# Performance work log

Measured on AMD Instinct MI355X. Metric: run time of the kernel, lower is better.

Reference implementation:

```python
import jax, jax.numpy as jnp
import numpy as np
import math

L, B, E, H = 1024, 4, 1024, 16
HD = E // H

def setup_inputs() -> dict:
    key = jax.random.key(0)
    ks = jax.random.split(key, 8)
    bound_in = math.sqrt(6.0 / (3 * E + E))  # xavier_uniform for [3E, E]
    bound_out = math.sqrt(1.0 / E)           # default Linear init
    return {
        "query": jax.random.normal(ks[0], (L, B, E), jnp.float32),
        "key": jax.random.normal(ks[1], (L, B, E), jnp.float32),
        "value": jax.random.normal(ks[2], (L, B, E), jnp.float32),
        "attn_mask": jnp.zeros((B, L, L), jnp.float32),
        "in_proj_weight": jax.random.uniform(ks[3], (3 * E, E), jnp.float32, -bound_in, bound_in),
        "in_proj_bias": jnp.zeros((3 * E,), jnp.float32),
        "out_proj_weight": jax.random.uniform(ks[4], (E, E), jnp.float32, -bound_out, bound_out),
        "out_proj_bias": jnp.zeros((E,), jnp.float32),
    }

def reference(query, key, value, attn_mask, in_proj_weight, in_proj_bias,
              out_proj_weight, out_proj_bias):
    # packed in-projection: q/k/v [L, B, E]
    q = query @ in_proj_weight[:E].T + in_proj_bias[:E]
    k = key @ in_proj_weight[E:2 * E].T + in_proj_bias[E:2 * E]
    v = value @ in_proj_weight[2 * E:].T + in_proj_bias[2 * E:]
    # [L, B, E] -> [B*H, L, HD]
    def to_heads(x):
        return x.reshape(L, B * H, HD).transpose(1, 0, 2)
    qh, kh, vh = to_heads(q), to_heads(k), to_heads(v)
    qh = qh / math.sqrt(HD)
    scores = jnp.einsum('bqd,bkd->bqk', qh, kh)  # [B*H, L, L]
    # per-batch mask repeated across heads: [B,L,L] -> [B*H,L,L]
    mask = jnp.repeat(attn_mask, H, axis=0)
    weights = jax.nn.softmax(scores + mask, axis=-1)
    out = jnp.einsum('bqk,bkd->bqd', weights, vh)  # [B*H, L, HD]
    out = out.transpose(1, 0, 2).reshape(L, B, E)
    attn_output = out @ out_proj_weight.T + out_proj_bias
    avg_weights = weights.reshape(B, H, L, L).mean(axis=1)
    return attn_output, avg_weights
```

## Files before the change

kernel.cpp:

```cpp
#include <hip/hip_runtime.h>
#include <hip/hip_bf16.h>
#include <cstdint>
#include <cstddef>

#define LL 1024
#define BB 4
#define EE 1024
#define HH 16
#define HD 64
#define NHEADS 64

typedef __bf16 bf16x8 __attribute__((ext_vector_type(8)));
typedef float f32x4 __attribute__((ext_vector_type(4)));
typedef unsigned short u16;
typedef unsigned char u8;

__device__ __forceinline__ u16 f2b(float f) {
  union { float f; unsigned int i; } v; v.f = f;
  unsigned int r = v.i + 0x7FFFu + ((v.i >> 16) & 1u);
  return (u16)(r >> 16);
}
__device__ __forceinline__ float fp8sel(unsigned int m4, int sel) {
  return __builtin_amdgcn_cvt_f32_fp8((int)(m4 >> (sel * 8)), 0);
}

__device__ __forceinline__ void gload16(const u16* g, u16* l) {
  __builtin_amdgcn_global_load_lds(
      (const __attribute__((address_space(1))) unsigned int*)(const void*)g,
      (__attribute__((address_space(3))) unsigned int*)(void*)l, 16, 0, 0);
}

#define CVT_TOTAL 5242880
__global__ __launch_bounds__(256)
void cvt_all(const float* __restrict__ q, const float* __restrict__ k,
             const float* __restrict__ v, const float* __restrict__ wi,
             const float* __restrict__ wo, const float* __restrict__ mask,
             u16* __restrict__ qb, u16* __restrict__ kb, u16* __restrict__ vb,
             u16* __restrict__ wib, u16* __restrict__ wob,
             unsigned int* __restrict__ emask) {
  int i = blockIdx.x * 256 + threadIdx.x;
  if (i >= CVT_TOTAL) return;
  if (i >= 4194304) {
    int off = i - 4194304;
    int l15 = off & 15, chunk = (off >> 4) & 15, bq = off >> 8;
    const float* mrow = mask + (size_t)bq * 1024 + chunk * 64 + l15;
    float e0 = __expf(mrow[0]);
    float e1 = __expf(mrow[16]);
    float e2 = __expf(mrow[32]);
    float e3 = __expf(mrow[48]);
    int lo = __builtin_amdgcn_cvt_pk_fp8_f32(e0, e1, 0, false);
    int vv = __builtin_amdgcn_cvt_pk_fp8_f32(e2, e3, lo, true);
    emask[(size_t)(bq * 16 + chunk) * 16 + l15] = (unsigned int)vv;
    return;
  }
  const float* s; u16* d; int off;
  if (i < 1048576)      { s = q;  d = qb;  off = i; }
  else if (i < 2097152) { s = k;  d = kb;  off = i - 1048576; }
  else if (i < 3145728) { s = v;  d = vb;  off = i - 2097152; }
  else if (i < 3932160) { s = wi; d = wib; off = i - 3145728; }
  else                  { s = wo; d = wob; off = i - 3932160; }
  const float4 t = ((const float4*)s)[off];
  u16 o[4] = { f2b(t.x), f2b(t.y), f2b(t.z), f2b(t.w) };
  *(uint2*)&d[(size_t)off * 4] = *(const uint2*)o;
}

__global__ __launch_bounds__(512, 6)
void gemm_in(const u16* __restrict__ A0, const u16* __restrict__ A1,
             const u16* __restrict__ A2, const u16* __restrict__ Bw,
             const float* __restrict__ bias,
             u16* __restrict__ Oq, u16* __restrict__ Ok, u16* __restrict__ Ov) {
  const int tid  = threadIdx.x;
  const int lane = tid & 63;
  const int wave = tid >> 6;
  const int quad = lane >> 4;
  const int l15  = lane & 15;
  const int wm = wave >> 1, wn = wave & 1;
  const int row0 = blockIdx.x * 128;
  const int col0 = blockIdx.y * 128;

  const int sec = col0 >> 10;
  const u16* A = (sec == 0) ? A0 : ((sec == 1) ? A1 : A2);

  __shared__ __align__(16) u16 lA[3][128][4][8];
  __shared__ __align__(16) u16 lB[3][128][4][8];

  f32x4 acc[2][4];
#pragma unroll
  for (int i = 0; i < 2; ++i)
#pragma unroll
    for (int j = 0; j < 4; ++j) { acc[i][j][0]=0.f; acc[i][j][1]=0.f; acc[i][j][2]=0.f; acc[i][j][3]=0.f; }

  auto stage = [&](int k0, int sbuf) {
    int r = tid >> 2, gs = tid & 3;
    int gg = gs ^ ((r >> 1) & 3);
    gload16(A  + (size_t)(row0 + r) * EE + (k0 + (gg << 3)), &lA[sbuf][0][0][0] + tid * 8);
    gload16(Bw + (size_t)(col0 + r) * EE + (k0 + (gg << 3)), &lB[sbuf][0][0][0] + tid * 8);
  };

  auto compute = [&](int cbuf) {
    const int gslot = quad ^ ((l15 >> 1) & 3);
    bf16x8 af[2], bfr[4];
#pragma unroll
    for (int i = 0; i < 2; ++i) af[i]  = *(const bf16x8*)&lA[cbuf][wm * 32 + i * 16 + l15][gslot][0];
#pragma unroll
    for (int j = 0; j < 4; ++j) bfr[j] = *(const bf16x8*)&lB[cbuf][wn * 64 + j * 16 + l15][gslot][0];
#pragma unroll
    for (int i = 0; i < 2; ++i)
#pragma unroll
      for (int j = 0; j < 4; ++j)
        acc[i][j] = __builtin_amdgcn_mfma_f32_16x16x32_bf16(af[i], bfr[j], acc[i][j], 0, 0, 0);
  };

  stage(0, 0);
  stage(32, 1);

  for (int it = 0; it < 31; ++it) {
    asm volatile("s_waitcnt vmcnt(2)" ::: "memory");
    __builtin_amdgcn_s_barrier();
    __builtin_amdgcn_sched_barrier(0);
    if (it < 30) stage((it + 2) * 32, (it + 2) % 3);
    compute(it % 3);
  }
  asm volatile("s_waitcnt vmcnt(0)" ::: "memory");
  __builtin_amdgcn_s_barrier();
  __builtin_amdgcn_sched_barrier(0);
  compute(31 % 3);

#pragma unroll
  for (int i = 0; i < 2; ++i) {
    const int grb = row0 + wm * 32 + i * 16 + quad * 4;
#pragma unroll
    for (int j = 0; j < 4; ++j) {
      const int gc = col0 + wn * 64 + j * 16 + l15;
      const float bv = bias[gc];
#pragma unroll
      for (int r = 0; r < 4; ++r) {
        float val = acc[i][j][r] + bv;
        const int gr = grb + r;
        const int l = gr >> 2, b = gr & 3;
        const int e = gc & 1023;
        const int h = e >> 6, d = e & 63;
        const int n = b * 16 + h;
        if (sec == 0)      Oq[((size_t)n * LL + l) * HD + d] = f2b(val * 0.125f);
        else if (sec == 1) Ok[((size_t)n * LL + l) * HD + d] = f2b(val);
        else               Ov[((size_t)n * HD + d) * LL + l] = f2b(val);
      }
    }
  }
}

__global__ __launch_bounds__(256, 4)
void gemm_out(const u16* __restrict__ A, const u16* __restrict__ Bw,
              const float* __restrict__ bias, float* __restrict__ Of) {
  const int tid  = threadIdx.x;
  const int lane = tid & 63;
  const int wave = tid >> 6;
  const int quad = lane >> 4;
  const int l15  = lane & 15;
  const int wm = wave >> 1, wn = wave & 1;
  const int row0 = blockIdx.x * 64;
  const int col0 = blockIdx.y * 64;

  __shared__ __align__(16) u16 lA[3][64][4][8];
  __shared__ __align__(16) u16 lB[3][64][4][8];

  f32x4 acc[2][2];
#pragma unroll
  for (int i = 0; i < 2; ++i)
#pragma unroll
    for (int j = 0; j < 2; ++j) { acc[i][j][0]=0.f; acc[i][j][1]=0.f; acc[i][j][2]=0.f; acc[i][j][3]=0.f; }

  auto stage = [&](int k0, int sbuf) {
    int r = tid >> 2, gs = tid & 3;
    int gg = gs ^ ((r >> 1) & 3);
    gload16(A  + (size_t)(row0 + r) * EE + (k0 + (gg << 3)), &lA[sbuf][0][0][0] + tid * 8);
    gload16(Bw + (size_t)(col0 + r) * EE + (k0 + (gg << 3)), &lB[sbuf][0][0][0] + tid * 8);
  };

  auto compute = [&](int cbuf) {
    const int gslot = quad ^ ((l15 >> 1) & 3);
    bf16x8 af[2], bfr[2];
#pragma unroll
    for (int i = 0; i < 2; ++i) af[i]  = *(const bf16x8*)&lA[cbuf][wm * 32 + i * 16 + l15][gslot][0];
#pragma unroll
    for (int j = 0; j < 2; ++j) bfr[j] = *(const bf16x8*)&lB[cbuf][wn * 32 + j * 16 + l15][gslot][0];
#pragma unroll
    for (int i = 0; i < 2; ++i)
#pragma unroll
      for (int j = 0; j < 2; ++j)
        acc[i][j] = __builtin_amdgcn_mfma_f32_16x16x32_bf16(af[i], bfr[j], acc[i][j], 0, 0, 0);
  };

  stage(0, 0);
  stage(32, 1);

  for (int it = 0; it < 31; ++it) {
    asm volatile("s_waitcnt vmcnt(2)" ::: "memory");
    __builtin_amdgcn_s_barrier();
    __builtin_amdgcn_sched_barrier(0);
    if (it < 30) stage((it + 2) * 32, (it + 2) % 3);
    compute(it % 3);
  }
  asm volatile("s_waitcnt vmcnt(0)" ::: "memory");
  __builtin_amdgcn_s_barrier();
  __builtin_amdgcn_sched_barrier(0);
  compute(31 % 3);

#pragma unroll
  for (int i = 0; i < 2; ++i) {
    const int grb = row0 + wm * 32 + i * 16 + quad * 4;
#pragma unroll
    for (int j = 0; j < 2; ++j) {
      const int gc = col0 + wn * 32 + j * 16 + l15;
      const float bv = bias[gc];
#pragma unroll
      for (int r = 0; r < 4; ++r)
        Of[(size_t)(grb + r) * EE + gc] = acc[i][j][r] + bv;
    }
  }
}

__global__ __launch_bounds__(512, 4)
void attn_fused(const u16* __restrict__ Qh, const u16* __restrict__ Kh,
                const u16* __restrict__ Vt, const u8* __restrict__ emask,
                float* __restrict__ rsbuf, u16* __restrict__ O) {
  const int tid = threadIdx.x, lane = tid & 63, wave = tid >> 6;
  const int quad = lane >> 4, l15 = lane & 15;
  const int n = blockIdx.x;
  const int q0 = blockIdx.y * 128;
  const int b = n >> 4, h = n & 15;
  const int qw = wave * 16;

  __shared__ __align__(16) u16 lQ[8][128][8];
  __shared__ __align__(16) u16 lK[2][8][64][8];
  __shared__ __align__(16) u16 lV[2][8][64][8];
  __shared__ __align__(16) u16 lW[128][72];

  const u16* Qb = Qh + ((size_t)n * LL + q0) * HD;
  const u16* Kb = Kh + (size_t)n * LL * HD;
  const u16* Vb = Vt + (size_t)n * HD * LL;
  const unsigned int* em32 = (const unsigned int*)emask;

#pragma unroll
  for (int p = 0; p < 2; ++p) {
    int lc = p * 512 + tid;
    gload16(Qb + (lc & 127) * HD + ((lc >> 7) << 3), &lQ[0][0][0] + lc * 8);
  }
  gload16(Kb + (size_t)(tid & 63) * HD + ((tid >> 6) << 3), &lK[0][0][0][0] + tid * 8);
  gload16(Vb + (size_t)(tid & 63) * LL + ((tid >> 6) << 3),  &lV[0][0][0][0] + tid * 8);
  __syncthreads();

  bf16x8 aq0 = *(const bf16x8*)&lQ[quad][qw + l15][0];
  bf16x8 aq1 = *(const bf16x8*)&lQ[4 + quad][qw + l15][0];

  float sr[4] = {0.f,0.f,0.f,0.f};
  f32x4 ctx[4];
#pragma unroll
  for (int j = 0; j < 4; ++j) { ctx[j][0]=0.f; ctx[j][1]=0.f; ctx[j][2]=0.f; ctx[j][3]=0.f; }

  int buf = 0;
  for (int kc = 0; kc < 16; ++kc) {
    if (kc < 15) {
      gload16(Kb + (size_t)((kc + 1) * 64 + (tid & 63)) * HD + ((tid >> 6) << 3),
              &lK[buf ^ 1][0][0][0] + tid * 8);
      gload16(Vb + (size_t)(tid & 63) * LL + (kc + 1) * 64 + ((tid >> 6) << 3),
              &lV[buf ^ 1][0][0][0] + tid * 8);
    }

    f32x4 sc[4];
#pragma unroll
    for (int jk = 0; jk < 4; ++jk) {
      bf16x8 bk0 = *(const bf16x8*)&lK[buf][quad][jk * 16 + l15][0];
      bf16x8 bk1 = *(const bf16x8*)&lK[buf][4 + quad][jk * 16 + l15][0];
      f32x4 a; a[0]=0.f; a[1]=0.f; a[2]=0.f; a[3]=0.f;
      a = __builtin_amdgcn_mfma_f32_16x16x32_bf16(aq0, bk0, a, 0, 0, 0);
      a = __builtin_amdgcn_mfma_f32_16x16x32_bf16(aq1, bk1, a, 0, 0, 0);
      sc[jk] = a;
    }
#pragma unroll
    for (int r = 0; r < 4; ++r) {
      const int q = q0 + qw + quad * 4 + r;
      const unsigned int m4 = em32[(((size_t)b * 1024 + q) * 16 + kc) * 16 + l15];
      float md[4];
      md[0] = __builtin_amdgcn_cvt_f32_fp8((int)m4, 0);
      md[1] = __builtin_amdgcn_cvt_f32_fp8((int)m4, 1);
      md[2] = __builtin_amdgcn_cvt_f32_fp8((int)m4, 2);
      md[3] = __builtin_amdgcn_cvt_f32_fp8((int)m4, 3);
      float ss = 0.0f;
#pragma unroll
      for (int jk = 0; jk < 4; ++jk) {
        float w = md[jk] * __expf(sc[jk][r]);
        ss += w;
        lW[qw + quad * 4 + r][jk * 16 + l15] = f2b(w);
      }
      sr[r] += ss;
    }

#pragma unroll
    for (int ks = 0; ks < 2; ++ks) {
      bf16x8 aw = *(const bf16x8*)&lW[qw + l15][ks * 32 + quad * 8];
#pragma unroll
      for (int j = 0; j < 4; ++j) {
        bf16x8 bv = *(const bf16x8*)&lV[buf][ks * 4 + quad][j * 16 + l15][0];
        ctx[j] = __builtin_amdgcn_mfma_f32_16x16x32_bf16(aw, bv, ctx[j], 0, 0, 0);
      }
    }

    __syncthreads();
    buf ^= 1;
  }

  float rs[4];
#pragma unroll
  for (int i = 0; i < 4; ++i) {
#pragma unroll
    for (int d = 1; d < 16; d <<= 1) sr[i] += __shfl_xor(sr[i], d);
    rs[i] = 1.0f / sr[i];
  }
#pragma unroll
  for (int j = 0; j < 4; ++j) {
    const int d = j * 16 + l15;
#pragma unroll
    for (int r = 0; r < 4; ++r) {
      const int l = q0 + qw + quad * 4 + r;
      O[((size_t)l * BB + b) * EE + h * 64 + d] = f2b(ctx[j][r] * rs[r]);
    }
  }
  if (l15 == 0) {
#pragma unroll
    for (int r = 0; r < 4; ++r) {
      const int q = q0 + qw + quad * 4 + r;
      rsbuf[n * LL + q] = rs[r];
    }
  }
}

__global__ __launch_bounds__(256, 2)
void attn_avg(const u16* __restrict__ Qh, const u16* __restrict__ Kh,
              const u8* __restrict__ emask, const float* __restrict__ rsbuf,
              float* __restrict__ avgout) {
  const int tid = threadIdx.x, lane = tid & 63, wave = tid >> 6;
  const int quad = lane >> 4, l15 = lane & 15;
  const int kc = blockIdx.x;
  const int q0 = blockIdx.y * 64;
  const int b = blockIdx.z;

  __shared__ __align__(16) u16 lQ[2][8][64][8];
  __shared__ __align__(16) u16 lK[2][8][128][8];

  float acc[8][4];
#pragma unroll
  for (int j = 0; j < 8; ++j)
#pragma unroll
    for (int r = 0; r < 4; ++r) acc[j][r] = 0.0f;

  const int qrb = q0 + wave * 16;
  const unsigned int* em32 = (const unsigned int*)emask;

  {
    const int n0 = b * 16;
    const u16* Qb = Qh + ((size_t)n0 * LL + q0) * HD;
    const u16* Kb = Kh + ((size_t)n0 * LL + kc * 128) * HD;
#pragma unroll
    for (int p = 0; p < 2; ++p) {
      int lc = p * 256 + tid;
      gload16(Qb + (lc & 63) * HD + ((lc >> 6) << 3), &lQ[0][0][0][0] + lc * 8);
    }
#pragma unroll
    for (int p = 0; p < 4; ++p) {
      int lc = p * 256 + tid;
      gload16(Kb + (size_t)(lc & 127) * HD + ((lc >> 7) << 3), &lK[0][0][0][0] + lc * 8);
    }
  }

  for (int h = 0; h < 16; ++h) {
    const int buf = h & 1;
    __syncthreads();
    if (h < 15) {
      const int n1 = b * 16 + h + 1;
      const u16* Qb = Qh + ((size_t)n1 * LL + q0) * HD;
      const u16* Kb = Kh + ((size_t)n1 * LL + kc * 128) * HD;
#pragma unroll
      for (int p = 0; p < 2; ++p) {
        int lc = p * 256 + tid;
        gload16(Qb + (lc & 63) * HD + ((lc >> 6) << 3), &lQ[buf ^ 1][0][0][0] + lc * 8);
      }
#pragma unroll
      for (int p = 0; p < 4; ++p) {
        int lc = p * 256 + tid;
        gload16(Kb + (size_t)(lc & 127) * HD + ((lc >> 7) << 3), &lK[buf ^ 1][0][0][0] + lc * 8);
      }
    }

    const int n = b * 16 + h;
    float rs[4];
#pragma unroll
    for (int r = 0; r < 4; ++r) {
      const int q = qrb + quad * 4 + r;
      rs[r] = rsbuf[n * LL + q];
    }
    bf16x8 aq0 = *(const bf16x8*)&lQ[buf][quad][wave * 16 + l15][0];
    bf16x8 aq1 = *(const bf16x8*)&lQ[buf][4 + quad][wave * 16 + l15][0];
#pragma unroll
    for (int j = 0; j < 8; ++j) {
      bf16x8 bk0 = *(const bf16x8*)&lK[buf][quad][j * 16 + l15][0];
      bf16x8 bk1 = *(const bf16x8*)&lK[buf][4 + quad][j * 16 + l15][0];
      f32x4 a; a[0]=0.f; a[1]=0.f; a[2]=0.f; a[3]=0.f;
      a = __builtin_amdgcn_mfma_f32_16x16x32_bf16(aq0, bk0, a, 0, 0, 0);
      a = __builtin_amdgcn_mfma_f32_16x16x32_bf16(aq1, bk1, a, 0, 0, 0);
#pragma unroll
      for (int r = 0; r < 4; ++r) acc[j][r] += __expf(a[r]) * rs[r];
    }
  }
#pragma unroll
  for (int j = 0; j < 8; ++j) {
    const int chunk = (kc << 1) + (j >> 2);
#pragma unroll
    for (int r = 0; r < 4; ++r) {
      const int q = qrb + quad * 4 + r;
      const int k = kc * 128 + j * 16 + l15;
      const unsigned int m4 = em32[(((size_t)b * 1024 + q) * 16 + chunk) * 16 + l15];
      const size_t idx = ((size_t)b << 20) + (size_t)q * LL + k;
      avgout[idx] = acc[j][r] * 0.0625f * fp8sel(m4, j & 3);
    }
  }
}

extern "C" void kernel_launch(void* const* d_in, const int* in_sizes, int n_in,
                              void* d_out, int out_size, void* d_ws, size_t ws_size,
                              hipStream_t stream) {
  const float* query = (const float*)d_in[0];
  const float* key   = (const float*)d_in[1];
  const float* value = (const float*)d_in[2];
  const float* mask  = (const float*)d_in[3];
  const float* win   = (const float*)d_in[4];
  const float* bin   = (const float*)d_in[5];
  const float* wout  = (const float*)d_in[6];
  const float* bout  = (const float*)d_in[7];
  float* out = (float*)d_out;

  u16* qb    = (u16*)d_ws;
  u16* kb    = qb + (size_t)LL * BB * EE;
  u16* vb    = kb + (size_t)LL * BB * EE;
  u16* winb  = vb + (size_t)LL * BB * EE;
  u16* woutb = winb + (size_t)3 * EE * EE;
  u16* Qh = woutb + (size_t)EE * EE;
  u16* Kh = Qh + (size_t)NHEADS * LL * HD;
  u16* Vt = Kh + (size_t)NHEADS * LL * HD;
  u16* O  = Vt + (size_t)NHEADS * LL * HD;
  float* rsbuf = (float*)(O + (size_t)LL * BB * EE);
  u8* emask = (u8*)(rsbuf + NHEADS * LL);

  dim3 blk(256);
  cvt_all<<<dim3((CVT_TOTAL + 255) / 256), blk, 0, stream>>>(
      query, key, value, win, wout, mask, qb, kb, vb, winb, woutb,
      (unsigned int*)emask);
  gemm_in<<<dim3(32, 24), dim3(512), 0, stream>>>(qb, kb, vb, winb, bin, Qh, Kh, Vt);
  attn_fused<<<dim3(64, 8), dim3(512), 0, stream>>>(Qh, Kh, Vt, emask, rsbuf, O);
  attn_avg<<<dim3(8, 16, 4), blk, 0, stream>>>(Qh, Kh, emask, rsbuf, out + (size_t)LL * BB * EE);
  gemm_out<<<dim3(64, 16), blk, 0, stream>>>(O, woutb, bout, out);
}
```

Baseline: 254.1 us.

## Fuse fp32-to-bf16 activation conversion into input projection GEMM staging

Removes the separate conversion pass for query/key/value. The input GEMM now reads fp32 activations directly through registers, converts them to bf16 and writes them to LDS, while weights still use direct global-to-LDS loads. This avoids writing and re-reading 24MB of bf16 intermediates. In exchange, each A tile is read at twice the byte count, the same activation rows are re-read across 8 column blocks per section, the pipeline now waits on vmcnt(0) each iteration, and register pressure rises.

```diff
diff --git a/kernel.cpp b/kernel.cpp
--- a/kernel.cpp
+++ b/kernel.cpp
@@ -30,18 +30,16 @@
       (__attribute__((address_space(3))) unsigned int*)(void*)l, 16, 0, 0);
 }
 
-#define CVT_TOTAL 5242880
+#define CVT_TOTAL 2097152
 __global__ __launch_bounds__(256)
-void cvt_all(const float* __restrict__ q, const float* __restrict__ k,
-             const float* __restrict__ v, const float* __restrict__ wi,
-             const float* __restrict__ wo, const float* __restrict__ mask,
-             u16* __restrict__ qb, u16* __restrict__ kb, u16* __restrict__ vb,
+void cvt_all(const float* __restrict__ wi, const float* __restrict__ wo,
+             const float* __restrict__ mask,
              u16* __restrict__ wib, u16* __restrict__ wob,
              unsigned int* __restrict__ emask) {
   int i = blockIdx.x * 256 + threadIdx.x;
   if (i >= CVT_TOTAL) return;
-  if (i >= 4194304) {
-    int off = i - 4194304;
+  if (i >= 1048576) {
+    int off = i - 1048576;
     int l15 = off & 15, chunk = (off >> 4) & 15, bq = off >> 8;
     const float* mrow = mask + (size_t)bq * 1024 + chunk * 64 + l15;
     float e0 = __expf(mrow[0]);
@@ -54,19 +52,16 @@
     return;
   }
   const float* s; u16* d; int off;
-  if (i < 1048576)      { s = q;  d = qb;  off = i; }
-  else if (i < 2097152) { s = k;  d = kb;  off = i - 1048576; }
-  else if (i < 3145728) { s = v;  d = vb;  off = i - 2097152; }
-  else if (i < 3932160) { s = wi; d = wib; off = i - 3145728; }
-  else                  { s = wo; d = wob; off = i - 3932160; }
+  if (i < 786432) { s = wi; d = wib; off = i; }
+  else            { s = wo; d = wob; off = i - 786432; }
   const float4 t = ((const float4*)s)[off];
   u16 o[4] = { f2b(t.x), f2b(t.y), f2b(t.z), f2b(t.w) };
   *(uint2*)&d[(size_t)off * 4] = *(const uint2*)o;
 }
 
 __global__ __launch_bounds__(512, 6)
-void gemm_in(const u16* __restrict__ A0, const u16* __restrict__ A1,
-             const u16* __restrict__ A2, const u16* __restrict__ Bw,
+void gemm_in(const float* __restrict__ A0, const float* __restrict__ A1,
+             const float* __restrict__ A2, const u16* __restrict__ Bw,
              const float* __restrict__ bias,
              u16* __restrict__ Oq, u16* __restrict__ Ok, u16* __restrict__ Ov) {
   const int tid  = threadIdx.x;
@@ -79,7 +74,7 @@
   const int col0 = blockIdx.y * 128;
 
   const int sec = col0 >> 10;
-  const u16* A = (sec == 0) ? A0 : ((sec == 1) ? A1 : A2);
+  const float* A = (sec == 0) ? A0 : ((sec == 1) ? A1 : A2);
 
   __shared__ __align__(16) u16 lA[3][128][4][8];
   __shared__ __align__(16) u16 lB[3][128][4][8];
@@ -90,11 +85,21 @@
 #pragma unroll
     for (int j = 0; j < 4; ++j) { acc[i][j][0]=0.f; acc[i][j][1]=0.f; acc[i][j][2]=0.f; acc[i][j][3]=0.f; }
 
-  auto stage = [&](int k0, int sbuf) {
-    int r = tid >> 2, gs = tid & 3;
-    int gg = gs ^ ((r >> 1) & 3);
-    gload16(A  + (size_t)(row0 + r) * EE + (k0 + (gg << 3)), &lA[sbuf][0][0][0] + tid * 8);
-    gload16(Bw + (size_t)(col0 + r) * EE + (k0 + (gg << 3)), &lB[sbuf][0][0][0] + tid * 8);
+  const int sr_ = tid >> 2, sgs = tid & 3;
+  const int sgg = sgs ^ ((sr_ >> 1) & 3);
+
+  float4 a0, a1;
+
+  auto stage_load = [&](int k0, int sbuf) {
+    const float* ap = A + (size_t)(row0 + sr_) * EE + (k0 + (sgg << 3));
+    a0 = *(const float4*)ap;
+    a1 = *(const float4*)(ap + 4);
+    gload16(Bw + (size_t)(col0 + sr_) * EE + (k0 + (sgg << 3)), &lB[sbuf][0][0][0] + tid * 8);
+  };
+  auto stage_write = [&](int sbuf) {
+    u16 o[8] = { f2b(a0.x), f2b(a0.y), f2b(a0.z), f2b(a0.w),
+                 f2b(a1.x), f2b(a1.y), f2b(a1.z), f2b(a1.w) };
+    *(uint4*)&lA[sbuf][sr_][sgs][0] = *(const uint4*)o;
   };
 
   auto compute = [&](int cbuf) {
@@ -111,20 +116,19 @@
         acc[i][j] = __builtin_amdgcn_mfma_f32_16x16x32_bf16(af[i], bfr[j], acc[i][j], 0, 0, 0);
   };
 
-  stage(0, 0);
-  stage(32, 1);
-
-  for (int it = 0; it < 31; ++it) {
-    asm volatile("s_waitcnt vmcnt(2)" ::: "memory");
+  stage_load(0, 0);
+  asm volatile("s_waitcnt vmcnt(0)" ::: "memory");
+  stage_write(0);
+  stage_load(32, 1);
+
+  for (int it = 0; it < 32; ++it) {
+    asm volatile("s_waitcnt vmcnt(0) lgkmcnt(0)" ::: "memory");
     __builtin_amdgcn_s_barrier();
     __builtin_amdgcn_sched_barrier(0);
-    if (it < 30) stage((it + 2) * 32, (it + 2) % 3);
+    if (it < 31) stage_write((it + 1) % 3);
+    if (it < 30) stage_load((it + 2) * 32, (it + 2) % 3);
     compute(it % 3);
   }
-  asm volatile("s_waitcnt vmcnt(0)" ::: "memory");
-  __builtin_amdgcn_s_barrier();
-  __builtin_amdgcn_sched_barrier(0);
-  compute(31 % 3);
 
 #pragma unroll
   for (int i = 0; i < 2; ++i) {
@@ -453,9 +457,8 @@
 
   dim3 blk(256);
   cvt_all<<<dim3((CVT_TOTAL + 255) / 256), blk, 0, stream>>>(
-      query, key, value, win, wout, mask, qb, kb, vb, winb, woutb,
-      (unsigned int*)emask);
-  gemm_in<<<dim3(32, 24), dim3(512), 0, stream>>>(qb, kb, vb, winb, bin, Qh, Kh, Vt);
+      win, wout, mask, winb, woutb, (unsigned int*)emask);
+  gemm_in<<<dim3(32, 24), dim3(512), 0, stream>>>(query, key, value, winb, bin, Qh, Kh, Vt);
   attn_fused<<<dim3(64, 8), dim3(512), 0, stream>>>(Qh, Kh, Vt, emask, rsbuf, O);
   attn_avg<<<dim3(8, 16, 4), blk, 0, stream>>>(Qh, Kh, emask, rsbuf, out + (size_t)LL * BB * EE);
   gemm_out<<<dim3(64, 16), blk, 0, stream>>>(O, woutb, bout, out);
```

After: 272.6 us. 7.2% more time.
